# Kernel tuning notes

Measured on AMD Instinct MI355X. Metric: run time of the kernel, lower is better.

Reference implementation:

```python
import jax, jax.numpy as jnp
import numpy as np

# Geometry from the hard-coded `options` tensor
VIEWS, DETS = 160, 640
H, W = 416, 416
D_IMG = 0.006641            # image pixel size
D_DET = 0.012858            # detector bin size
ANG0 = 0.0
D_ANG = 0.009817477 * 4     # = 2*pi/160 (full scan)
S2R = 5.95                  # source-to-rotation-center distance
D2R = 4.906                 # detector-to-rotation-center distance
VIRDET = D_DET * S2R / (S2R + D2R)   # detector rescaled to isocenter (virtual detector)
PI = float(np.pi)
COEF = PI / VIEWS
BATCH = 32


def setup_inputs() -> dict:
    key = jax.random.key(0)
    projection = jax.random.normal(key, (BATCH, 1, VIEWS, DETS), dtype=jnp.float32)

    # Ramp filter (Ram-Lak, spatial domain), length 2*dets-1, exactly as in torch __init__
    x = np.arange(2 * DETS - 1) - DETS + 1
    x_safe = np.where(x == 0, 1, x).astype(np.float64)
    filt = np.where(np.abs(x) % 2 == 1,
                    -1.0 / (PI * PI * x_safe * x_safe * VIRDET * VIRDET),
                    0.0)
    filt[x == 0] = 1.0 / (4.0 * VIRDET * VIRDET)
    filt = jnp.asarray(filt.reshape(1, 1, 1, -1), dtype=jnp.float32)

    # Cosine (fan-beam) pre-weighting, detector bin centers at (i - dets/2 + 0.5)*virdet
    u = (np.arange(DETS) - DETS / 2 + 0.5) * VIRDET
    wv = S2R / np.sqrt(S2R ** 2 + u ** 2) * VIRDET
    w = jnp.asarray(wv.reshape(1, 1, 1, -1), dtype=jnp.float32)

    return {"projection": projection, "w": w, "filt": filt}


def _backproject(p):
    """Pixel-driven equidistant fan-beam backprojection.
    p: filtered sinogram [B, 1, VIEWS, DETS] -> recon [B, 1, H, W].
    """
    betas = ANG0 + D_ANG * jnp.arange(VIEWS, dtype=jnp.float32)
    xs = (jnp.arange(W, dtype=jnp.float32) - (W - 1) / 2.0) * D_IMG   # [W]
    ys = ((H - 1) / 2.0 - jnp.arange(H, dtype=jnp.float32)) * D_IMG   # [H]
    Xg, Yg = jnp.meshgrid(xs, ys)   # both [H, W]

    pv = jnp.moveaxis(p, 2, 0)  # [VIEWS, B, 1, DETS]

    def step(acc, inp):
        beta, pb = inp                      # pb: [B, 1, DETS]
        cb, sb = jnp.cos(beta), jnp.sin(beta)
        d = Xg * cb + Yg * sb               # pixel component toward source
        r = -Xg * sb + Yg * cb              # perpendicular component
        U = S2R - d                         # source-to-pixel depth
        # detector coordinate at isocenter -> fractional bin index
        idx = (S2R * r / U) / VIRDET + (DETS - 1) / 2.0   # [H, W]
        valid = (idx >= 0.0) & (idx <= DETS - 1)
        i0 = jnp.clip(jnp.floor(idx), 0, DETS - 2).astype(jnp.int32)
        frac = jnp.clip(idx - i0.astype(jnp.float32), 0.0, 1.0)
        # irregular gather + linear interpolation: [B,1,H,W]
        v = pb[:, :, i0] * (1.0 - frac) + pb[:, :, i0 + 1] * frac
        wgt = jnp.where(valid, (S2R / U) ** 2, 0.0)       # distance weighting
        return acc + wgt * v, None

    init = jnp.zeros((p.shape[0], 1, H, W), dtype=p.dtype)
    acc, _ = jax.lax.scan(step, init, (betas, pv))
    return acc


def reference(projection, w, filt):
    # 1) cosine weighting (elementwise broadcast over detector axis)
    p = projection * w
    p = jax.lax.conv_general_dilated(
        p, filt, window_strides=(1, 1),
        padding=((0, 0), (DETS - 1, DETS - 1)),
        dimension_numbers=("NCHW", "OIHW", "NCHW"))
    # 3) geometric backprojection + angular step normalization
    return COEF * _backproject(p)
```

## Files before the change

kernel.cpp:

```cpp
#include <hip/hip_runtime.h>

#define VIEWS 160
#define DETS  640
#define H_IMG 416
#define W_IMG 416
#define BATCH 32

constexpr double D_IMG_D  = 0.006641;
constexpr double D_DET_D  = 0.012858;
constexpr double S2R_D    = 5.95;
constexpr double D2R_D    = 4.906;
constexpr double VIRDET_D = D_DET_D * S2R_D / (S2R_D + D2R_D);
constexpr double PI_D     = 3.14159265358979323846;

typedef __fp16 __attribute__((ext_vector_type(2))) h2f;

#define TILES_X 13
#define TILES_Y 52
#define NTILES  (TILES_X * TILES_Y)
#define NB      64
#define ZSPLIT  3

__global__ __launch_bounds__(256) void init_kernel(float* __restrict__ vcs,
                                                   int* __restrict__ bs_tab,
                                                   float4* __restrict__ out4) {
    int t    = threadIdx.x;
    int tile = blockIdx.x;
    if (t < VIEWS) {
        int v = t;
        float dang = (float)(0.009817477 * 4.0);
        float beta = dang * (float)v;
        float cb = cosf(beta), sb = sinf(beta);
        float K  = (float)(S2R_D / VIRDET_D);
        if (tile == 0) {
            ((float4*)vcs)[v] = make_float4(cb, sb, -K * sb, K * cb);
        }
        int ty = tile / TILES_X, tx = tile - ty * TILES_X;
        float XL = ((float)(tx * 32) - 207.5f) * (float)D_IMG_D;
        float XR = ((float)(tx * 32 + 31) - 207.5f) * (float)D_IMG_D;
        float YT = (207.5f - (float)(ty * 8)) * (float)D_IMG_D;
        float YB = (207.5f - (float)(ty * 8 + 7)) * (float)D_IMG_D;
        float m = 1e30f;
#define CORNER(Xc, Yc) { \
        float r_ = -(Xc) * sb + (Yc) * cb; \
        float U_ = (float)S2R_D - (Xc) * cb - (Yc) * sb; \
        float ix = fmaf(K, r_ / U_, 319.5f); \
        m = fminf(m, ix); }
        CORNER(XL, YT); CORNER(XR, YT); CORNER(XL, YB); CORNER(XR, YB);
#undef CORNER
        int bs = (int)floorf(m) - 2;
        bs = max(0, min(DETS - NB, bs)) & ~1;
        bs_tab[tile * VIEWS + v] = bs;
    }
    size_t base = (size_t)tile * 2048 + t;
    float4 z = make_float4(0.f, 0.f, 0.f, 0.f);
    #pragma unroll
    for (int i = 0; i < 8; ++i) out4[base + (size_t)i * 256] = z;
}

#define FT 320
#define RPAD 24
#define RSTR 209
__global__ __launch_bounds__(FT) void filter_kernel(
    const float* __restrict__ proj, const float* __restrict__ w,
    const float* __restrict__ filt, unsigned int* __restrict__ pf) {
    __shared__ float4 s_in[4 * RSTR];
    __shared__ float  s_f[2 * DETS];
    __shared__ unsigned int s_out[2 * DETS];

    int t = threadIdx.x;
    int g = blockIdx.x;
    int group4 = g / 160;
    int v = g - group4 * 160;

    for (int e = t; e < 4 * RSTR; e += FT) {
        int ri = e / RSTR, c4 = e - ri * RSTR;
        float4 pv = make_float4(0.f, 0.f, 0.f, 0.f);
        if (c4 >= RPAD && c4 < RPAD + 160) {
            int b = group4 * 4 + ri;
            pv = ((const float4*)(proj + ((size_t)b * VIEWS + v) * DETS))[c4 - RPAD];
            float4 wv = ((const float4*)w)[c4 - RPAD];
            pv.x *= wv.x; pv.y *= wv.y; pv.z *= wv.z; pv.w *= wv.w;
        }
        s_in[e] = pv;
    }
    for (int e = t; e < 2 * DETS; e += FT) s_f[e] = (e < 2 * DETS - 1) ? filt[e] : 0.f;
    __syncthreads();

    int sub = (t >= 160) ? 1 : 0;
    int tj  = t - sub * 160;

    const float4* f4  = (const float4*)s_f;
    const float4* in4 = &s_in[sub * 2 * RSTR + tj];
    float4 o0 = {0,0,0,0}, o1 = {0,0,0,0};
    float4 fp = f4[135];
    #pragma unroll 2
    for (int u = 0; u < 50; ++u) {
        float4 fn = f4[136 + u];
        {
            float4 iv = in4[0 * RSTR + u];
            o0.x = fmaf(iv.x, fp.w, o0.x); o0.x = fmaf(iv.y, fn.x, o0.x);
            o0.x = fmaf(iv.z, fn.y, o0.x); o0.x = fmaf(iv.w, fn.z, o0.x);
            o0.y = fmaf(iv.x, fp.z, o0.y); o0.y = fmaf(iv.y, fp.w, o0.y);
            o0.y = fmaf(iv.z, fn.x, o0.y); o0.y = fmaf(iv.w, fn.y, o0.y);
            o0.z = fmaf(iv.x, fp.y, o0.z); o0.z = fmaf(iv.y, fp.z, o0.z);
            o0.z = fmaf(iv.z, fp.w, o0.z); o0.z = fmaf(iv.w, fn.x, o0.z);
            o0.w = fmaf(iv.x, fp.x, o0.w); o0.w = fmaf(iv.y, fp.y, o0.w);
            o0.w = fmaf(iv.z, fp.z, o0.w); o0.w = fmaf(iv.w, fp.w, o0.w);
        }
        {
            float4 iv = in4[1 * RSTR + u];
            o1.x = fmaf(iv.x, fp.w, o1.x); o1.x = fmaf(iv.y, fn.x, o1.x);
            o1.x = fmaf(iv.z, fn.y, o1.x); o1.x = fmaf(iv.w, fn.z, o1.x);
            o1.y = fmaf(iv.x, fp.z, o1.y); o1.y = fmaf(iv.y, fp.w, o1.y);
            o1.y = fmaf(iv.z, fn.x, o1.y); o1.y = fmaf(iv.w, fn.y, o1.y);
            o1.z = fmaf(iv.x, fp.y, o1.z); o1.z = fmaf(iv.y, fp.z, o1.z);
            o1.z = fmaf(iv.z, fp.w, o1.z); o1.z = fmaf(iv.w, fn.x, o1.z);
            o1.w = fmaf(iv.x, fp.x, o1.w); o1.w = fmaf(iv.y, fp.y, o1.w);
            o1.w = fmaf(iv.z, fp.z, o1.w); o1.w = fmaf(iv.w, fp.w, o1.w);
        }
        fp = fn;
    }

    float coef = (float)((PI_D / (double)VIEWS) * S2R_D * S2R_D);
    auto h0 = __builtin_amdgcn_cvt_pkrtz(o0.x * coef, o1.x * coef);
    auto h1 = __builtin_amdgcn_cvt_pkrtz(o0.y * coef, o1.y * coef);
    auto h2 = __builtin_amdgcn_cvt_pkrtz(o0.z * coef, o1.z * coef);
    auto h3 = __builtin_amdgcn_cvt_pkrtz(o0.w * coef, o1.w * coef);
    uint4 pk = make_uint4(__builtin_bit_cast(unsigned int, h0),
                          __builtin_bit_cast(unsigned int, h1),
                          __builtin_bit_cast(unsigned int, h2),
                          __builtin_bit_cast(unsigned int, h3));
    *(uint4*)&s_out[sub * DETS + 4 * tj] = pk;
    __syncthreads();

    unsigned int a0 = s_out[2 * t],        a1 = s_out[2 * t + 1];
    unsigned int b0 = s_out[DETS + 2 * t], b1 = s_out[DETS + 2 * t + 1];
    uint4 o = make_uint4(a0, b0, a1, b1);
    ((uint4*)(pf + ((size_t)v * 8 + group4) * (2 * DETS)))[t] = o;
}

__device__ __forceinline__ void gld_lds16(const char* g, char* l) {
    __builtin_amdgcn_global_load_lds(
        (const __attribute__((address_space(1))) unsigned int*)g,
        (__attribute__((address_space(3))) unsigned int*)l, 16, 0, 0);
}

__global__ __launch_bounds__(256, 8) void bp_kernel(
    const unsigned int* __restrict__ pf, const float* __restrict__ vcs,
    const int* __restrict__ bs_tab, float* __restrict__ out) {
    __shared__ alignas(16) unsigned int s_buf[2 * 1024];

    int t    = threadIdx.x;
    int zc   = blockIdx.z;
    int tile = blockIdx.y * TILES_X + blockIdx.x;
    int x    = blockIdx.x * 32 + (t & 31);
    int y    = blockIdx.y * 8 + (t >> 5);

    float X  = ((float)x - 207.5f) * (float)D_IMG_D;
    float Yv = (207.5f - (float)y) * (float)D_IMG_D;

    int vstart = (zc * VIEWS) / ZSPLIT;
    int vend   = ((zc + 1) * VIEWS) / ZSPLIT;
    int nv     = vend - vstart;
    const float4* vc4 = (const float4*)vcs + vstart;
    const int*    bsp = bs_tab + tile * VIEWS + vstart;
    const char*   pfb = (const char*)pf + (size_t)vstart * 40960;
    int  goff  = (t >> 5) * (DETS * 8) + (t & 31) * 16;
    int  ldoff = (t >> 6) << 10;

    float acc[32];
    #pragma unroll
    for (int b = 0; b < 32; ++b) acc[b] = 0.f;
    h2f hacc[16];
    #pragma unroll
    for (int p = 0; p < 16; ++p) hacc[p] = (h2f)0.f;

    #define STAGE(c) do { \
        int bsd = bsp[(c)]; \
        gld_lds16(pfb + (size_t)(c) * 40960 + (size_t)bsd * 8 + goff, \
                  (char*)s_buf + (((c) & 1) << 12) + ldoff); \
    } while (0)

    STAGE(0);
    __syncthreads();

    for (int c = 0; c < nv; ++c) {
        if (c + 1 < nv) STAGE(c + 1);

        float4 a  = vc4[c];
        int    bsc = bsp[c];
        float U   = fmaf(-X, a.x, fmaf(-Yv, a.y, (float)S2R_D));
        float num = fmaf(X, a.z, Yv * a.w);
        float ru   = __builtin_amdgcn_rcpf(U);
        float idx  = fmaf(num, ru, 319.5f);
        float idxc = __builtin_amdgcn_fmed3f(idx, 0.f, 639.f);
        float i0f  = fminf(idxc, 638.0f);
        int   i0   = (int)i0f;
        float frac = idxc - truncf(i0f);
        float w2   = ru * ru;
        float wgt  = (idx == idxc) ? w2 : 0.f;
        float w1f  = wgt * frac;
        float w0f  = wgt - w1f;
        h2f w0h = __builtin_amdgcn_cvt_pkrtz(w0f, w0f);
        h2f w1h = __builtin_amdgcn_cvt_pkrtz(w1f, w1f);
        int bl = min(max(i0 - bsc, 0), NB - 2);
        const uint2* L = (const uint2*)((const char*)s_buf + ((c & 1) << 12)) + bl;
        #pragma unroll
        for (int gg = 0; gg < 8; ++gg) {
            uint2 A = L[gg * NB];
            uint2 B = L[gg * NB + 1];
            h2f pa = __builtin_bit_cast(h2f, A.x);
            h2f pb = __builtin_bit_cast(h2f, B.x);
            h2f pc = __builtin_bit_cast(h2f, A.y);
            h2f pd = __builtin_bit_cast(h2f, B.y);
            hacc[2 * gg]     = __builtin_elementwise_fma(pa, w0h, hacc[2 * gg]);
            hacc[2 * gg]     = __builtin_elementwise_fma(pb, w1h, hacc[2 * gg]);
            hacc[2 * gg + 1] = __builtin_elementwise_fma(pc, w0h, hacc[2 * gg + 1]);
            hacc[2 * gg + 1] = __builtin_elementwise_fma(pd, w1h, hacc[2 * gg + 1]);
        }
        if ((c & 7) == 7) {
            #pragma unroll
            for (int gg = 0; gg < 8; ++gg) {
                acc[4 * gg + 0] += (float)hacc[2 * gg].x;
                acc[4 * gg + 1] += (float)hacc[2 * gg].y;
                acc[4 * gg + 2] += (float)hacc[2 * gg + 1].x;
                acc[4 * gg + 3] += (float)hacc[2 * gg + 1].y;
                hacc[2 * gg] = (h2f)0.f; hacc[2 * gg + 1] = (h2f)0.f;
            }
        }
        __syncthreads();
    }
    #undef STAGE

    #pragma unroll
    for (int gg = 0; gg < 8; ++gg) {
        acc[4 * gg + 0] += (float)hacc[2 * gg].x;
        acc[4 * gg + 1] += (float)hacc[2 * gg].y;
        acc[4 * gg + 2] += (float)hacc[2 * gg + 1].x;
        acc[4 * gg + 3] += (float)hacc[2 * gg + 1].y;
    }

    float* ob = out + (size_t)y * W_IMG + x;
    #pragma unroll
    for (int b = 0; b < 32; ++b)
        unsafeAtomicAdd(ob + (size_t)b * (H_IMG * W_IMG), acc[b]);
}

extern "C" void kernel_launch(void* const* d_in, const int* in_sizes, int n_in,
                              void* d_out, int out_size, void* d_ws, size_t ws_size,
                              hipStream_t stream) {
    const float* proj = (const float*)d_in[0];
    const float* w    = (const float*)d_in[1];
    const float* filt = (const float*)d_in[2];
    float* out = (float*)d_out;

    float*        vcs    = (float*)d_ws;
    int*          bs_tab = (int*)((char*)d_ws + 4096);
    unsigned int* pf     = (unsigned int*)((char*)d_ws + 4096 + 432640);

    init_kernel<<<NTILES, 256, 0, stream>>>(vcs, bs_tab, (float4*)out);
    filter_kernel<<<(BATCH / 4) * VIEWS, FT, 0, stream>>>(proj, w, filt, pf);
    bp_kernel<<<dim3(TILES_X, TILES_Y, ZSPLIT), 256, 0, stream>>>(pf, vcs, bs_tab, out);
}
```

Baseline: 190.7 us.

## Store filtered sinogram as interleaved neighbor pairs and accumulate with fdot2

The filter kernel now writes each detector bin packed with its right neighbor (i, i+1) across all batches, using a swizzled layout sized for 16-byte loads. The backprojection kernel does each bilinear interpolation as one fp16 dot2 into fp32 accumulators, which removes the fp16 partial accumulators and their periodic flushes. The z-split drops from 3 to 2, the LDS buffer doubles, and the launch-bounds occupancy hint drops from 8 to 6. This trades twice the sinogram traffic and LDS for fewer instructions and better accumulation precision.

```diff
diff --git a/kernel.cpp b/kernel.cpp
--- a/kernel.cpp
+++ b/kernel.cpp
@@ -19,7 +19,16 @@
 #define TILES_Y 52
 #define NTILES  (TILES_X * TILES_Y)
 #define NB      64
-#define ZSPLIT  3
+#define ZSPLIT  2
+
+
+__device__ __forceinline__ float dot2_acc(h2f p, h2f w, float acc) {
+#if __has_builtin(__builtin_amdgcn_fdot2)
+    return __builtin_amdgcn_fdot2(p, w, acc, false);
+#else
+    return fmaf((float)p.x, (float)w.x, fmaf((float)p.y, (float)w.y, acc));
+#endif
+}
 
 __global__ __launch_bounds__(256) void init_kernel(float* __restrict__ vcs,
                                                    int* __restrict__ bs_tab,
@@ -63,7 +72,7 @@
 #define RSTR 209
 __global__ __launch_bounds__(FT) void filter_kernel(
     const float* __restrict__ proj, const float* __restrict__ w,
-    const float* __restrict__ filt, unsigned int* __restrict__ pf) {
+    const float* __restrict__ filt, unsigned int* __restrict__ pf2) {
     __shared__ float4 s_in[4 * RSTR];
     __shared__ float  s_f[2 * DETS];
     __shared__ unsigned int s_out[2 * DETS];
@@ -134,10 +143,22 @@
     *(uint4*)&s_out[sub * DETS + 4 * tj] = pk;
     __syncthreads();
 
-    unsigned int a0 = s_out[2 * t],        a1 = s_out[2 * t + 1];
-    unsigned int b0 = s_out[DETS + 2 * t], b1 = s_out[DETS + 2 * t + 1];
-    uint4 o = make_uint4(a0, b0, a1, b1);
-    ((uint4*)(pf + ((size_t)v * 8 + group4) * (2 * DETS)))[t] = o;
+    unsigned int* dstv = pf2 + (size_t)v * 20480 + (size_t)group4 * 4;
+    #pragma unroll
+    for (int cc = 0; cc < 2; ++cc) {
+        int k  = 2 * t + cc;
+        int k1 = k + 1;
+        unsigned int u0  = s_out[k];
+        unsigned int u0n = (k1 < DETS) ? s_out[k1] : 0u;
+        unsigned int u1  = s_out[DETS + k];
+        unsigned int u1n = (k1 < DETS) ? s_out[DETS + k1] : 0u;
+        uint4 o;
+        o.x = __builtin_amdgcn_perm(u0n, u0, 0x05040100u);
+        o.y = __builtin_amdgcn_perm(u0n, u0, 0x07060302u);
+        o.z = __builtin_amdgcn_perm(u1n, u1, 0x05040100u);
+        o.w = __builtin_amdgcn_perm(u1n, u1, 0x07060302u);
+        *(uint4*)(dstv + (size_t)cc * 10240 + (size_t)t * 32) = o;
+    }
 }
 
 __device__ __forceinline__ void gld_lds16(const char* g, char* l) {
@@ -146,13 +167,13 @@
         (__attribute__((address_space(3))) unsigned int*)l, 16, 0, 0);
 }
 
-__global__ __launch_bounds__(256, 8) void bp_kernel(
-    const unsigned int* __restrict__ pf, const float* __restrict__ vcs,
+__global__ __launch_bounds__(256, 6) void bp_kernel(
+    const unsigned int* __restrict__ pf2, const float* __restrict__ vcs,
     const int* __restrict__ bs_tab, float* __restrict__ out) {
-    __shared__ alignas(16) unsigned int s_buf[2 * 1024];
+    __shared__ alignas(16) unsigned int s_buf[2 * 2048];
 
     int t    = threadIdx.x;
-    int zc   = blockIdx.z;
+    int half = blockIdx.z;
     int tile = blockIdx.y * TILES_X + blockIdx.x;
     int x    = blockIdx.x * 32 + (t & 31);
     int y    = blockIdx.y * 8 + (t >> 5);
@@ -160,38 +181,39 @@
     float X  = ((float)x - 207.5f) * (float)D_IMG_D;
     float Yv = (207.5f - (float)y) * (float)D_IMG_D;
 
-    int vstart = (zc * VIEWS) / ZSPLIT;
-    int vend   = ((zc + 1) * VIEWS) / ZSPLIT;
-    int nv     = vend - vstart;
+    int vstart = half * (VIEWS / ZSPLIT);
     const float4* vc4 = (const float4*)vcs + vstart;
     const int*    bsp = bs_tab + tile * VIEWS + vstart;
-    const char*   pfb = (const char*)pf + (size_t)vstart * 40960;
-    int  goff  = (t >> 5) * (DETS * 8) + (t & 31) * 16;
-    int  ldoff = (t >> 6) << 10;
+    const char*   pfb = (const char*)pf2 + (size_t)vstart * 81920;
+
+    int r_s  = (t >> 3) & 31;
+    int k_s  = t & 7;
+    int toff0 = r_s * 128 + ((k_s ^ (r_s & 7)) << 4);
+    int wvbase = (t >> 6) << 10;
 
     float acc[32];
     #pragma unroll
     for (int b = 0; b < 32; ++b) acc[b] = 0.f;
-    h2f hacc[16];
-    #pragma unroll
-    for (int p = 0; p < 16; ++p) hacc[p] = (h2f)0.f;
 
     #define STAGE(c) do { \
         int bsd = bsp[(c)]; \
-        gld_lds16(pfb + (size_t)(c) * 40960 + (size_t)bsd * 8 + goff, \
-                  (char*)s_buf + (((c) & 1) << 12) + ldoff); \
+        const char* src = pfb + (size_t)(c) * 81920 + (size_t)bsd * 64; \
+        char* dst = (char*)s_buf + (((c) & 1) << 13) + wvbase; \
+        gld_lds16(src + toff0, dst); \
+        gld_lds16(src + 40960 + toff0, dst + 4096); \
     } while (0)
 
     STAGE(0);
     __syncthreads();
 
+    int nv = VIEWS / ZSPLIT;
     for (int c = 0; c < nv; ++c) {
         if (c + 1 < nv) STAGE(c + 1);
 
-        float4 a  = vc4[c];
+        float4 a   = vc4[c];
         int    bsc = bsp[c];
-        float U   = fmaf(-X, a.x, fmaf(-Yv, a.y, (float)S2R_D));
-        float num = fmaf(X, a.z, Yv * a.w);
+        float U    = fmaf(-X, a.x, fmaf(-Yv, a.y, (float)S2R_D));
+        float num  = fmaf(X, a.z, Yv * a.w);
         float ru   = __builtin_amdgcn_rcpf(U);
         float idx  = fmaf(num, ru, 319.5f);
         float idxc = __builtin_amdgcn_fmed3f(idx, 0.f, 639.f);
@@ -202,44 +224,24 @@
         float wgt  = (idx == idxc) ? w2 : 0.f;
         float w1f  = wgt * frac;
         float w0f  = wgt - w1f;
-        h2f w0h = __builtin_amdgcn_cvt_pkrtz(w0f, w0f);
-        h2f w1h = __builtin_amdgcn_cvt_pkrtz(w1f, w1f);
-        int bl = min(max(i0 - bsc, 0), NB - 2);
-        const uint2* L = (const uint2*)((const char*)s_buf + ((c & 1) << 12)) + bl;
+        h2f w01    = __builtin_amdgcn_cvt_pkrtz(w0f, w1f);
+
+        int rel = min(max(i0 - bsc, 0), NB - 2);
+        int cc  = rel & 1;
+        int rr  = rel >> 1;
+        int b2  = ((c & 1) << 13) + (cc << 12) + (rr << 7) + ((rr & 7) << 4);
+        const char* pbase = (const char*)s_buf;
         #pragma unroll
-        for (int gg = 0; gg < 8; ++gg) {
-            uint2 A = L[gg * NB];
-            uint2 B = L[gg * NB + 1];
-            h2f pa = __builtin_bit_cast(h2f, A.x);
-            h2f pb = __builtin_bit_cast(h2f, B.x);
-            h2f pc = __builtin_bit_cast(h2f, A.y);
-            h2f pd = __builtin_bit_cast(h2f, B.y);
-            hacc[2 * gg]     = __builtin_elementwise_fma(pa, w0h, hacc[2 * gg]);
-            hacc[2 * gg]     = __builtin_elementwise_fma(pb, w1h, hacc[2 * gg]);
-            hacc[2 * gg + 1] = __builtin_elementwise_fma(pc, w0h, hacc[2 * gg + 1]);
-            hacc[2 * gg + 1] = __builtin_elementwise_fma(pd, w1h, hacc[2 * gg + 1]);
-        }
-        if ((c & 7) == 7) {
-            #pragma unroll
-            for (int gg = 0; gg < 8; ++gg) {
-                acc[4 * gg + 0] += (float)hacc[2 * gg].x;
-                acc[4 * gg + 1] += (float)hacc[2 * gg].y;
-                acc[4 * gg + 2] += (float)hacc[2 * gg + 1].x;
-                acc[4 * gg + 3] += (float)hacc[2 * gg + 1].y;
-                hacc[2 * gg] = (h2f)0.f; hacc[2 * gg + 1] = (h2f)0.f;
-            }
+        for (int k = 0; k < 8; ++k) {
+            uint4 q = *(const uint4*)(pbase + (b2 ^ (k << 4)));
+            acc[4 * k + 0] = dot2_acc(__builtin_bit_cast(h2f, q.x), w01, acc[4 * k + 0]);
+            acc[4 * k + 1] = dot2_acc(__builtin_bit_cast(h2f, q.y), w01, acc[4 * k + 1]);
+            acc[4 * k + 2] = dot2_acc(__builtin_bit_cast(h2f, q.z), w01, acc[4 * k + 2]);
+            acc[4 * k + 3] = dot2_acc(__builtin_bit_cast(h2f, q.w), w01, acc[4 * k + 3]);
         }
         __syncthreads();
     }
     #undef STAGE
-
-    #pragma unroll
-    for (int gg = 0; gg < 8; ++gg) {
-        acc[4 * gg + 0] += (float)hacc[2 * gg].x;
-        acc[4 * gg + 1] += (float)hacc[2 * gg].y;
-        acc[4 * gg + 2] += (float)hacc[2 * gg + 1].x;
-        acc[4 * gg + 3] += (float)hacc[2 * gg + 1].y;
-    }
 
     float* ob = out + (size_t)y * W_IMG + x;
     #pragma unroll
@@ -257,9 +259,9 @@
 
     float*        vcs    = (float*)d_ws;
     int*          bs_tab = (int*)((char*)d_ws + 4096);
-    unsigned int* pf     = (unsigned int*)((char*)d_ws + 4096 + 432640);
+    unsigned int* pf2    = (unsigned int*)((char*)d_ws + 442368);
 
     init_kernel<<<NTILES, 256, 0, stream>>>(vcs, bs_tab, (float4*)out);
-    filter_kernel<<<(BATCH / 4) * VIEWS, FT, 0, stream>>>(proj, w, filt, pf);
-    bp_kernel<<<dim3(TILES_X, TILES_Y, ZSPLIT), 256, 0, stream>>>(pf, vcs, bs_tab, out);
-}
+    filter_kernel<<<(BATCH / 4) * VIEWS, FT, 0, stream>>>(proj, w, filt, pf2);
+    bp_kernel<<<dim3(TILES_X, TILES_Y, ZSPLIT), 256, 0, stream>>>(pf2, vcs, bs_tab, out);
+}
```

Measured after the change: 203.0 us. 1.06x slower.
